# Kernel optimization log

Measured on AMD Instinct MI355X. Metric: run time of the kernel, lower is better.

Reference implementation:

```python
import jax, jax.numpy as jnp
import numpy as np

NP_, NG_ = 20000, 5000            # protein / go_annotation node counts
D_FEAT, D_HID, N_CLS = 512, 128, 1000
E_PP, E_PG, E_GP = 240000, 100000, 100000
NEG_SLOPE = -0.2                  # note: the repo default slope is negative
EPS = 1e-12


def _l2norm(x):
    n = jnp.linalg.norm(x, axis=1, keepdims=True)
    return x / jnp.maximum(n, EPS)


def _edge_softmax(logits, dst, n):
    # per-destination-node softmax over incoming edges, per feature channel
    m = jax.ops.segment_max(logits, dst, num_segments=n)
    e = jnp.exp(logits - m[dst])
    s = jax.ops.segment_sum(e, dst, num_segments=n)
    return e / s[dst]


def _type_attn(h_src, h_dst, src, dst, Wl, bl, Wr, br):
    # GCN-normalized aggregation onto dst nodes, then type-level attention logits,
    # broadcast back to edges (copy_u on the reversed relation graph).
    ns, nd = h_src.shape[0], h_dst.shape[0]
    ones = jnp.ones(src.shape[0], dtype=h_src.dtype)
    outdeg = jnp.clip(jax.ops.segment_sum(ones, src, num_segments=ns), 1.0)
    feat = h_src * (outdeg ** -0.5)[:, None]
    rst = jax.ops.segment_sum(feat[src], dst, num_segments=nd)
    indeg = jnp.clip(jax.ops.segment_sum(ones, dst, num_segments=nd), 1.0)
    rst = rst * (indeg ** -0.5)[:, None]
    ea = jax.nn.elu((h_dst @ Wl + bl) + (rst @ Wr + br))  # [nd, D_HID]
    return ea[dst]                                        # [E, D_HID]


def setup_inputs() -> dict:
    key = jax.random.key(0)
    ks = iter(jax.random.split(key, 40))

    def nrm(shape, s=0.05):
        return jax.random.normal(next(ks), shape, dtype=jnp.float32) * s

    def ri(n, hi):
        return jax.random.randint(next(ks), (n,), 0, hi, dtype=jnp.int32)

    zeros = lambda n: jnp.zeros((n,), jnp.float32)
    return dict(
        x_protein=jax.random.normal(next(ks), (NP_, D_FEAT), dtype=jnp.float32),
        x_go=jax.random.normal(next(ks), (NG_, N_CLS), dtype=jnp.float32),
        src_pp=ri(E_PP, NP_), dst_pp=ri(E_PP, NP_),
        src_pg=ri(E_PG, NP_), dst_pg=ri(E_PG, NG_),
        src_gp=ri(E_GP, NG_), dst_gp=ri(E_GP, NP_),
        W1p=nrm((D_FEAT, D_HID)), b1p=zeros(D_HID),
        W1g=nrm((N_CLS, D_HID)), b1g=zeros(D_HID),
        Wl_p=nrm((D_HID, D_HID)), bl_p=zeros(D_HID),
        Wl_g=nrm((D_HID, D_HID)), bl_g=zeros(D_HID),
        Wr_p=nrm((D_HID, D_HID)), br_p=zeros(D_HID),
        Wr_g=nrm((D_HID, D_HID)), br_g=zeros(D_HID),
        Wnl=nrm((D_HID, D_HID)), bnl=zeros(D_HID),
        Wnr=nrm((D_HID, D_HID)), bnr=zeros(D_HID),
        Wfc=nrm((D_HID, N_CLS)), bfc=zeros(N_CLS),
    )


def reference(x_protein, x_go, src_pp, dst_pp, src_pg, dst_pg, src_gp, dst_gp,
              W1p, b1p, W1g, b1g, Wl_p, bl_p, Wl_g, bl_g,
              Wr_p, br_p, Wr_g, br_g, Wnl, bnl, Wnr, bnr, Wfc, bfc):
    # input projection + row-wise l2 norm (dropout disabled / eval mode)
    hp = _l2norm(x_protein @ W1p + b1p)   # [NP, D_HID]
    hg = _l2norm(x_go @ W1g + b1g)        # [NG, D_HID]

    # ---- TypeAttention over each canonical etype ----
    a_pp = _type_attn(hp, hp, src_pp, dst_pp, Wl_p, bl_p, Wr_p, br_p)
    a_pg = _type_attn(hp, hg, src_pg, dst_pg, Wl_g, bl_g, Wr_p, br_p)
    a_gp = _type_attn(hg, hp, src_gp, dst_gp, Wl_p, bl_p, Wr_g, br_g)

    # homogeneous view: proteins [0,NP), go_annotation [NP,NP+NG)
    gsrc = jnp.concatenate([src_pp, src_pg, src_gp + NP_])
    gdst = jnp.concatenate([dst_pp, dst_pg + NP_, dst_gp])
    alpha = jnp.concatenate([a_pp, a_pg, a_gp], axis=0)   # [E, D_HID]
    n = NP_ + NG_
    alpha = _edge_softmax(alpha, gdst, n)

    # ---- NodeAttention on the homogeneous graph ----
    x = jnp.concatenate([hp, hg], axis=0)                 # [N, D_HID]
    hl = (x @ Wnl + bnl)[gsrc]
    hr = (x @ Wnr + bnr)[gdst]
    e = (hl + hr) * alpha
    e = jnp.where(e > 0, e, NEG_SLOPE * e)                # LeakyReLU(slope=-0.2)
    a = _edge_softmax(e, gdst, n)
    h = jax.ops.segment_sum(x[gsrc] * a, gdst, num_segments=n)

    out = h @ Wfc + bfc   # [N, N_CLS]; rows [:NP]=protein, [NP:]=go_annotation
    return out
```

## Files before the change

### kernel.cpp

```cpp
#include <hip/hip_runtime.h>
#include <math.h>

#define NP 20000
#define NG 5000
#define NTOT 25000
#define DF 512
#define NCLS 1000
#define DH 128
#define EPP 240000
#define EPG 100000
#define EGP 100000
#define ETOT 440000

typedef __attribute__((ext_vector_type(8))) __bf16 bf16x8;
typedef __attribute__((ext_vector_type(4))) float f32x4;

__device__ __forceinline__ void gl2lds16(const void* g, void* l) {
    __builtin_amdgcn_global_load_lds(
        (const __attribute__((address_space(1))) unsigned int*)g,
        (__attribute__((address_space(3))) unsigned int*)l, 16, 0, 0);
}

__device__ __forceinline__ float b2f(unsigned short u) {
    union { unsigned int i; float f; } c; c.i = ((unsigned int)u) << 16; return c.f;
}

__global__ void hist_kernel(const int* __restrict__ src_pp, const int* __restrict__ dst_pp,
                            const int* __restrict__ src_pg, const int* __restrict__ dst_pg,
                            const int* __restrict__ src_gp, const int* __restrict__ dst_gp,
                            int* outdeg_pp, int* outdeg_pg, int* outdeg_gp,
                            int* indeg_pp, int* indeg_gp, int* indeg_pg,
                            int* cnt)
{
    int e = blockIdx.x * blockDim.x + threadIdx.x;
    if (e < EPP) {
        int s = src_pp[e], d = dst_pp[e];
        atomicAdd(&outdeg_pp[s], 1); atomicAdd(&indeg_pp[d], 1); atomicAdd(&cnt[d], 1);
    } else if (e < EPP + EPG) {
        int i = e - EPP; int s = src_pg[i], d = dst_pg[i];
        atomicAdd(&outdeg_pg[s], 1); atomicAdd(&indeg_pg[d], 1); atomicAdd(&cnt[NP + d], 1);
    } else if (e < ETOT) {
        int i = e - EPP - EPG; int s = src_gp[i], d = dst_gp[i];
        atomicAdd(&outdeg_gp[s], 1); atomicAdd(&indeg_gp[d], 1); atomicAdd(&cnt[d], 1);
    }
}

__global__ __launch_bounds__(1024) void scan_kernel(const int* __restrict__ cnt, int* __restrict__ row_ptr)
{
    __shared__ int part[1024];
    int t = threadIdx.x;
    const int CH = (NTOT + 1023) / 1024;
    int base = t * CH;
    int s = 0;
    for (int i = 0; i < CH; i++) { int idx = base + i; if (idx < NTOT) s += cnt[idx]; }
    part[t] = s;
    __syncthreads();
    for (int off = 1; off < 1024; off <<= 1) {
        int v = (t >= off) ? part[t - off] : 0;
        __syncthreads();
        part[t] += v;
        __syncthreads();
    }
    int run = (t == 0) ? 0 : part[t - 1];
    for (int i = 0; i < CH; i++) {
        int idx = base + i;
        if (idx < NTOT) { row_ptr[idx] = run; run += cnt[idx]; }
    }
    if (t == 1023) row_ptr[NTOT] = part[1023];
}

__global__ void scatter_kernel(const int* __restrict__ src_pp, const int* __restrict__ dst_pp,
                               const int* __restrict__ src_pg, const int* __restrict__ dst_pg,
                               const int* __restrict__ src_gp, const int* __restrict__ dst_gp,
                               const int* __restrict__ outdeg_pp, const int* __restrict__ outdeg_pg,
                               const int* __restrict__ outdeg_gp,
                               const int* __restrict__ row_ptr, int* fill,
                               int* __restrict__ payload, float* __restrict__ escale)
{
    int e = blockIdx.x * blockDim.x + threadIdx.x;
    int s, d, t; float sc;
    if (e < EPP) {
        s = src_pp[e]; d = dst_pp[e]; t = 0;
        sc = rsqrtf((float)max(outdeg_pp[s], 1));
    } else if (e < EPP + EPG) {
        int i = e - EPP; s = src_pg[i]; d = NP + dst_pg[i]; t = 1;
        sc = rsqrtf((float)max(outdeg_pg[s], 1));
    } else if (e < ETOT) {
        int i = e - EPP - EPG; int sl = src_gp[i]; s = NP + sl; d = dst_gp[i]; t = 2;
        sc = rsqrtf((float)max(outdeg_gp[sl], 1));
    } else return;
    int pos = row_ptr[d] + atomicAdd(&fill[d], 1);
    payload[pos] = s | (t << 16);
    escale[pos] = sc;
}

__global__ __launch_bounds__(256) void conv_x_kernel(const float* __restrict__ xp, const float* __restrict__ xg,
                                                     __bf16* __restrict__ xpb, __bf16* __restrict__ xgb)
{
    long long e = ((long long)blockIdx.x * 256 + threadIdx.x) * 8;
    __bf16 pk[8];
    if (blockIdx.y == 0) {
        if (e >= (long long)20032 * 512) return;
        int row = (int)(e >> 9), k = (int)(e & 511);
        if (row < NP) {
            f32x4 v0 = *(const f32x4*)(xp + (size_t)row * 512 + k);
            f32x4 v1 = *(const f32x4*)(xp + (size_t)row * 512 + k + 4);
#pragma unroll
            for (int i = 0; i < 4; i++) { pk[i] = (__bf16)v0[i]; pk[4 + i] = (__bf16)v1[i]; }
        } else {
#pragma unroll
            for (int i = 0; i < 8; i++) pk[i] = (__bf16)0.f;
        }
        *(bf16x8*)(xpb + e) = *(bf16x8*)pk;
    } else {
        if (e >= (long long)5056 * 1024) return;
        int row = (int)(e >> 10), k = (int)(e & 1023);
        if (row < NG && k + 7 < 1000) {
            f32x4 v0 = *(const f32x4*)(xg + (size_t)row * 1000 + k);
            f32x4 v1 = *(const f32x4*)(xg + (size_t)row * 1000 + k + 4);
#pragma unroll
            for (int i = 0; i < 4; i++) { pk[i] = (__bf16)v0[i]; pk[4 + i] = (__bf16)v1[i]; }
        } else {
#pragma unroll
            for (int i = 0; i < 8; i++) {
                int kk = k + i;
                pk[i] = (__bf16)((row < NG && kk < 1000) ? xg[(size_t)row * 1000 + kk] : 0.f);
            }
        }
        *(bf16x8*)(xgb + e) = *(bf16x8*)pk;
    }
}

__global__ __launch_bounds__(256) void conv_w_kernel(
    const float* W1p, const float* W1g, const float* Wlp, const float* Wrp, const float* Wrg,
    const float* Wnl, const float* Wnr, const float* Wfc,
    __bf16* w1pt, __bf16* w1gt, __bf16* wlpt, __bf16* wrpt, __bf16* wrgt,
    __bf16* wnlt, __bf16* wnrt, __bf16* wfct)
{
    int e = blockIdx.x * 256 + threadIdx.x;
    switch (blockIdx.y) {
    case 0: if (e < 128 * 512)  { int n = e >> 9, k = e & 511;  w1pt[e] = (__bf16)W1p[(size_t)k * 128 + n]; } break;
    case 1: if (e < 128 * 1024) { int n = e >> 10, k = e & 1023; w1gt[e] = (__bf16)(k < 1000 ? W1g[(size_t)k * 128 + n] : 0.f); } break;
    case 2: if (e < 16384) { int n = e >> 7, k = e & 127; wlpt[e] = (__bf16)Wlp[(size_t)k * 128 + n]; } break;
    case 3: if (e < 16384) { int n = e >> 7, k = e & 127; wrpt[e] = (__bf16)Wrp[(size_t)k * 128 + n]; } break;
    case 4: if (e < 16384) { int n = e >> 7, k = e & 127; wrgt[e] = (__bf16)Wrg[(size_t)k * 128 + n]; } break;
    case 5: if (e < 16384) { int n = e >> 7, k = e & 127; wnlt[e] = (__bf16)Wnl[(size_t)k * 128 + n]; } break;
    case 6: if (e < 16384) { int n = e >> 7, k = e & 127; wnrt[e] = (__bf16)Wnr[(size_t)k * 128 + n]; } break;
    case 7: if (e < 1024 * 128) { int n = e >> 7, k = e & 127; wfct[e] = (__bf16)(n < 1000 ? Wfc[(size_t)k * 1000 + n] : 0.f); } break;
    }
}

struct GJob {
    const __bf16* A1; const __bf16* A2;
    const __bf16* B1; const __bf16* B2;
    const float* b1; const float* b2;
    float* O1; float* O2; __bf16* Ob;
    int M, N, Kp, ksteps;
};

template<int ACT, int DUALA, int DUALW, int EMIT>
__global__ __launch_bounds__(256) void gemm_bt(GJob j0, GJob j1, int split)
{
    __shared__ __align__(16) __bf16 As[64 * 32];
    __shared__ __align__(16) __bf16 A2s[DUALA ? 64 * 32 : 8];
    __shared__ __align__(16) __bf16 Bs[128 * 32];
    __shared__ __align__(16) __bf16 B2s[(DUALA || DUALW) ? 128 * 32 : 8];
    __shared__ float part[2][64];

    GJob j; int bx;
    if ((int)blockIdx.x < split) { j = j0; bx = blockIdx.x; }
    else { j = j1; bx = blockIdx.x - split; }

    const int tid = threadIdx.x;
    const int wave = tid >> 6, lane = tid & 63;
    const int wr = wave >> 1, wc = wave & 1;
    const int l15 = lane & 15, lh = lane >> 4;
    const int row0 = bx * 64;
    const int col0 = blockIdx.y * 128;

    const size_t aoff = (size_t)(row0 + (tid >> 2)) * j.Kp + (tid & 3) * 8;
    const size_t boff0 = (size_t)(col0 + (tid >> 2)) * j.Kp + (tid & 3) * 8;
    const size_t boff1 = boff0 + (size_t)64 * j.Kp;
    char* alds  = (char*)As + wave * 1024;
    char* a2lds = (char*)A2s + wave * 1024;
    char* blds0 = (char*)Bs + wave * 1024;
    char* blds1 = (char*)Bs + 4096 + wave * 1024;
    char* b2lds0 = (char*)B2s + wave * 1024;
    char* b2lds1 = (char*)B2s + 4096 + wave * 1024;

    f32x4 acc[2][4], acc2[2][4];
#pragma unroll
    for (int fm = 0; fm < 2; fm++)
#pragma unroll
        for (int fn = 0; fn < 4; fn++) {
            acc[fm][fn] = (f32x4)0.f;
            if (DUALW) acc2[fm][fn] = (f32x4)0.f;
        }

    for (int ks = 0; ks < j.ksteps; ks++) {
        const int k0 = ks * 32;
        __syncthreads();
        gl2lds16(j.A1 + aoff + k0, alds);
        if (DUALA) gl2lds16(j.A2 + aoff + k0, a2lds);
        gl2lds16(j.B1 + boff0 + k0, blds0);
        gl2lds16(j.B1 + boff1 + k0, blds1);
        if (DUALA || DUALW) {
            gl2lds16(j.B2 + boff0 + k0, b2lds0);
            gl2lds16(j.B2 + boff1 + k0, b2lds1);
        }
        __syncthreads();

#pragma unroll
        for (int fm = 0; fm < 2; fm++) {
            bf16x8 a = *(const bf16x8*)&As[(wr * 32 + fm * 16 + l15) * 32 + lh * 8];
            bf16x8 a2;
            if (DUALA) a2 = *(const bf16x8*)&A2s[(wr * 32 + fm * 16 + l15) * 32 + lh * 8];
#pragma unroll
            for (int fn = 0; fn < 4; fn++) {
                bf16x8 b = *(const bf16x8*)&Bs[(wc * 64 + fn * 16 + l15) * 32 + lh * 8];
                acc[fm][fn] = __builtin_amdgcn_mfma_f32_16x16x32_bf16(a, b, acc[fm][fn], 0, 0, 0);
                if (DUALA) {
                    bf16x8 b2 = *(const bf16x8*)&B2s[(wc * 64 + fn * 16 + l15) * 32 + lh * 8];
                    acc[fm][fn] = __builtin_amdgcn_mfma_f32_16x16x32_bf16(a2, b2, acc[fm][fn], 0, 0, 0);
                }
                if (DUALW) {
                    bf16x8 b2 = *(const bf16x8*)&B2s[(wc * 64 + fn * 16 + l15) * 32 + lh * 8];
                    acc2[fm][fn] = __builtin_amdgcn_mfma_f32_16x16x32_bf16(a, b2, acc2[fm][fn], 0, 0, 0);
                }
            }
        }
    }

    float bias[4], bias2[4];
#pragma unroll
    for (int fn = 0; fn < 4; fn++) {
        int col = col0 + wc * 64 + fn * 16 + l15;
        bias[fn] = 0.f; bias2[fn] = 0.f;
        if (col < j.N) {
            bias[fn] = DUALA ? (j.b1[col] + j.b2[col]) : j.b1[col];
            if (DUALW) bias2[fn] = j.b2[col];
        }
    }

    float vv[2][4][4];
#pragma unroll
    for (int fm = 0; fm < 2; fm++)
#pragma unroll
        for (int fn = 0; fn < 4; fn++)
#pragma unroll
            for (int r = 0; r < 4; r++) {
                float v = acc[fm][fn][r] + bias[fn];
                if (ACT == 1) v = v > 0.f ? v : (expf(v) - 1.f);
                vv[fm][fn][r] = v;
            }

    float scale[2][4];
#pragma unroll
    for (int fm = 0; fm < 2; fm++)
#pragma unroll
        for (int r = 0; r < 4; r++) scale[fm][r] = 1.f;

    if (ACT == 2) {
        float s[2][4];
#pragma unroll
        for (int fm = 0; fm < 2; fm++)
#pragma unroll
            for (int r = 0; r < 4; r++) {
                float v = 0.f;
#pragma unroll
                for (int fn = 0; fn < 4; fn++) v += vv[fm][fn][r] * vv[fm][fn][r];
                v += __shfl_xor(v, 1);
                v += __shfl_xor(v, 2);
                v += __shfl_xor(v, 4);
                v += __shfl_xor(v, 8);
                s[fm][r] = v;
            }
        __syncthreads();
        if (l15 == 0) {
#pragma unroll
            for (int fm = 0; fm < 2; fm++)
#pragma unroll
                for (int r = 0; r < 4; r++)
                    part[wc][wr * 32 + fm * 16 + lh * 4 + r] = s[fm][r];
        }
        __syncthreads();
#pragma unroll
        for (int fm = 0; fm < 2; fm++)
#pragma unroll
            for (int r = 0; r < 4; r++) {
                int rl = wr * 32 + fm * 16 + lh * 4 + r;
                float ss = part[0][rl] + part[1][rl];
                scale[fm][r] = 1.f / fmaxf(sqrtf(ss), 1e-12f);
            }
    }

#pragma unroll
    for (int fm = 0; fm < 2; fm++)
#pragma unroll
        for (int fn = 0; fn < 4; fn++)
#pragma unroll
            for (int r = 0; r < 4; r++) {
                int row = row0 + wr * 32 + fm * 16 + lh * 4 + r;
                int col = col0 + wc * 64 + fn * 16 + l15;
                if (row < j.M && col < j.N) {
                    float v = vv[fm][fn][r] * scale[fm][r];
                    if (EMIT != 2) j.O1[(size_t)row * j.N + col] = v;
                    if (EMIT != 0) j.Ob[(size_t)row * j.N + col] = (__bf16)v;
                    if (DUALW) j.O2[(size_t)row * j.N + col] = acc2[fm][fn][r] + bias2[fn];
                }
            }
}

__global__ __launch_bounds__(128) void rst_agg_kernel(const __bf16* __restrict__ x,
                                                      const int* __restrict__ row_ptr,
                                                      const int* __restrict__ payload,
                                                      const float* __restrict__ escale,
                                                      const int* __restrict__ indeg_pp,
                                                      const int* __restrict__ indeg_gp,
                                                      __bf16* __restrict__ rppb, __bf16* __restrict__ rgpb)
{
    int d = blockIdx.x;
    int c = threadIdx.x;
    int beg = row_ptr[d], end = row_ptr[d + 1];
    float spp = 0.f, sgp = 0.f;
    __shared__ int pl[128];
    __shared__ float sc[128];
    const unsigned short* xu = (const unsigned short*)x;
    for (int base = beg; base < end; base += 128) {
        int n = min(128, end - base);
        __syncthreads();
        if (c < n) { pl[c] = payload[base + c]; sc[c] = escale[base + c]; }
        __syncthreads();
        for (int i = 0; i < n; i++) {
            int p = pl[i]; int s = p & 0xFFFF; int t = p >> 16;
            float v = b2f(xu[(size_t)s * DH + c]) * sc[i];
            if (t == 0) spp += v; else sgp += v;
        }
    }
    float ipp = rsqrtf((float)max(indeg_pp[d], 1));
    float igp = rsqrtf((float)max(indeg_gp[d], 1));
    rppb[(size_t)d * DH + c] = (__bf16)(spp * ipp);
    rgpb[(size_t)d * DH + c] = (__bf16)(sgp * igp);
}

__global__ void wa_kernel(const int* __restrict__ indeg_pp, const int* __restrict__ indeg_gp,
                          float* __restrict__ eapp, float* __restrict__ eagp)
{
    int idx = blockIdx.x * blockDim.x + threadIdx.x;
    if (idx >= NP * DH) return;
    int d = idx >> 7;
    int npp = indeg_pp[d], ngp = indeg_gp[d];
    float app = eapp[idx], agp = eagp[idx];
    float wpp = 0.f, wgp = 0.f;
    if (npp > 0 && ngp > 0) {
        float mx = fmaxf(app, agp);
        float epp = __expf(app - mx), egp = __expf(agp - mx);
        float den = (float)npp * epp + (float)ngp * egp;
        wpp = epp / den; wgp = egp / den;
    } else if (npp > 0) wpp = 1.f / (float)npp;
    else if (ngp > 0) wgp = 1.f / (float)ngp;
    eapp[idx] = wpp;
    eagp[idx] = wgp;
}

__global__ __launch_bounds__(128) void node_attn_kernel(const __bf16* __restrict__ x,
                                                        const __bf16* __restrict__ hlb,
                                                        const float* __restrict__ hr,
                                                        const float* __restrict__ wpp_arr, const float* __restrict__ wgp_arr,
                                                        const int* __restrict__ indeg_pg,
                                                        const int* __restrict__ row_ptr, const int* __restrict__ payload,
                                                        __bf16* __restrict__ hb)
{
    int d = blockIdx.x, c = threadIdx.x;
    int beg = row_ptr[d], end = row_ptr[d + 1];
    float hrd = hr[(size_t)d * DH + c];
    float wpp = 0.f, wgp = 0.f;
    if (d < NP) {
        wpp = wpp_arr[(size_t)d * DH + c];
        wgp = wgp_arr[(size_t)d * DH + c];
    } else {
        float wpg = 1.f / (float)max(indeg_pg[d - NP], 1);
        wpp = wpg; wgp = wpg;
    }
    float ssum = 0.f, acc = 0.f;
    __shared__ int pl[128];
    const unsigned short* xu = (const unsigned short*)x;
    const unsigned short* hu = (const unsigned short*)hlb;
    for (int base = beg; base < end; base += 128) {
        int n = min(128, end - base);
        __syncthreads();
        if (c < n) pl[c] = payload[base + c];
        __syncthreads();
        for (int i = 0; i < n; i++) {
            int p = pl[i]; int s = p & 0xFFFF; int t = p >> 16;
            float al = (t == 0) ? wpp : wgp;
            float e = (b2f(hu[(size_t)s * DH + c]) + hrd) * al;
            e = fmaxf(e, -0.2f * e);
            float pw = __expf(e);
            float xv = b2f(xu[(size_t)s * DH + c]);
            ssum += pw;
            acc += pw * xv;
        }
    }
    hb[(size_t)d * DH + c] = (__bf16)((end > beg) ? acc / ssum : 0.f);
}

extern "C" void kernel_launch(void* const* d_in, const int* in_sizes, int n_in,
                              void* d_out, int out_size, void* d_ws, size_t ws_size,
                              hipStream_t stream)
{
    const float* x_protein = (const float*)d_in[0];
    const float* x_go      = (const float*)d_in[1];
    const int* src_pp = (const int*)d_in[2];
    const int* dst_pp = (const int*)d_in[3];
    const int* src_pg = (const int*)d_in[4];
    const int* dst_pg = (const int*)d_in[5];
    const int* src_gp = (const int*)d_in[6];
    const int* dst_gp = (const int*)d_in[7];
    const float* W1p = (const float*)d_in[8];
    const float* b1p = (const float*)d_in[9];
    const float* W1g = (const float*)d_in[10];
    const float* b1g = (const float*)d_in[11];
    const float* Wl_p = (const float*)d_in[12];
    const float* bl_p = (const float*)d_in[13];
    const float* Wr_p = (const float*)d_in[16];
    const float* br_p = (const float*)d_in[17];
    const float* Wr_g = (const float*)d_in[18];
    const float* br_g = (const float*)d_in[19];
    const float* Wnl = (const float*)d_in[20];
    const float* bnl = (const float*)d_in[21];
    const float* Wnr = (const float*)d_in[22];
    const float* bnr = (const float*)d_in[23];
    const float* Wfc = (const float*)d_in[24];
    const float* bfc = (const float*)d_in[25];
    float* out = (float*)d_out;

    size_t off = 0;
    char* base = (char*)d_ws;
    auto alloc = [&](size_t words) { void* p = base + off * 4; off += (words + 7) & ~(size_t)7; return p; };

    __bf16* xb   = (__bf16*)alloc((size_t)25024 * 128 / 2);
    float*  hr   = (float*)alloc((size_t)25000 * 128);
    __bf16* hlb  = (__bf16*)alloc((size_t)25024 * 128 / 2);
    __bf16* rppb = (__bf16*)alloc((size_t)20032 * 128 / 2);
    __bf16* rgpb = (__bf16*)alloc((size_t)20032 * 128 / 2);
    char* R1 = (char*)alloc((size_t)5128192 + 2588672);
    __bf16* xpb = (__bf16*)R1;
    __bf16* xgb = (__bf16*)(R1 + (size_t)20032 * 512 * 2);
    float*  wpp = (float*)R1;
    float*  wgp = wpp + (size_t)20000 * 128;
    __bf16* haggb = (__bf16*)(wgp + (size_t)20000 * 128);
    __bf16* w1pt = (__bf16*)alloc(128 * 512 / 2);
    __bf16* w1gt = (__bf16*)alloc(128 * 1024 / 2);
    __bf16* wlpt = (__bf16*)alloc(128 * 128 / 2);
    __bf16* wrpt = (__bf16*)alloc(128 * 128 / 2);
    __bf16* wrgt = (__bf16*)alloc(128 * 128 / 2);
    __bf16* wnlt = (__bf16*)alloc(128 * 128 / 2);
    __bf16* wnrt = (__bf16*)alloc(128 * 128 / 2);
    __bf16* wfct = (__bf16*)alloc(1024 * 128 / 2);
    int* ibase = (int*)alloc(140000 + 25001 + 440000);
    int* outdeg_pp = ibase;
    int* outdeg_pg = outdeg_pp + NP;
    int* outdeg_gp = outdeg_pg + NP;
    int* indeg_pp  = outdeg_gp + NG;
    int* indeg_gp  = indeg_pp + NP;
    int* indeg_pg  = indeg_gp + NP;
    int* cnt       = indeg_pg + NG;
    int* fill      = cnt + NTOT;
    int* row_ptr   = fill + NTOT;
    int* payload   = row_ptr + NTOT + 1;
    float* escale  = (float*)alloc(440000);

    hipMemsetAsync(ibase, 0, (size_t)140000 * sizeof(int), stream);

    const int EB = (ETOT + 255) / 256;
    hist_kernel<<<EB, 256, 0, stream>>>(src_pp, dst_pp, src_pg, dst_pg, src_gp, dst_gp,
                                        outdeg_pp, outdeg_pg, outdeg_gp,
                                        indeg_pp, indeg_gp, indeg_pg, cnt);
    scan_kernel<<<1, 1024, 0, stream>>>(cnt, row_ptr);
    scatter_kernel<<<EB, 256, 0, stream>>>(src_pp, dst_pp, src_pg, dst_pg, src_gp, dst_gp,
                                           outdeg_pp, outdeg_pg, outdeg_gp,
                                           row_ptr, fill, payload, escale);

    conv_x_kernel<<<dim3(5008, 2), 256, 0, stream>>>(x_protein, x_go, xpb, xgb);
    conv_w_kernel<<<dim3(512, 8), 256, 0, stream>>>(W1p, W1g, Wl_p, Wr_p, Wr_g, Wnl, Wnr, Wfc,
                                                    w1pt, w1gt, wlpt, wrpt, wrgt, wnlt, wnrt, wfct);

    {
        GJob p0 = { xpb, nullptr, w1pt, nullptr, b1p, nullptr, nullptr, nullptr, xb, NP, 128, 512, 16 };
        GJob p1 = { xgb, nullptr, w1gt, nullptr, b1g, nullptr, nullptr, nullptr,
                    xb + (size_t)NP * 128, NG, 128, 1024, 32 };
        gemm_bt<2, 0, 0, 2><<<392, 256, 0, stream>>>(p0, p1, 313);
    }

    rst_agg_kernel<<<NP, 128, 0, stream>>>(xb, row_ptr, payload, escale, indeg_pp, indeg_gp, rppb, rgpb);

    {
        GJob e0 = { xb, rppb, wlpt, wrpt, bl_p, br_p, wpp, nullptr, nullptr, NP, 128, 128, 4 };
        GJob e1 = { xb, rgpb, wlpt, wrgt, bl_p, br_g, wgp, nullptr, nullptr, NP, 128, 128, 4 };
        gemm_bt<1, 1, 0, 0><<<626, 256, 0, stream>>>(e0, e1, 313);
    }

    wa_kernel<<<(NP * DH + 255) / 256, 256, 0, stream>>>(indeg_pp, indeg_gp, wpp, wgp);

    {
        GJob h0 = { xb, nullptr, wnlt, wnrt, bnl, bnr, nullptr, hr, hlb, NTOT, 128, 128, 4 };
        gemm_bt<0, 0, 1, 2><<<391, 256, 0, stream>>>(h0, h0, 1 << 30);
    }

    node_attn_kernel<<<NTOT, 128, 0, stream>>>(xb, hlb, hr, wpp, wgp, indeg_pg, row_ptr, payload, haggb);

    {
        GJob o0 = { haggb, nullptr, wfct, nullptr, bfc, nullptr, out, nullptr, nullptr, NTOT, NCLS, 128, 4 };
        gemm_bt<0, 0, 0, 0><<<dim3(391, 8), 256, 0, stream>>>(o0, o0, 1 << 30);
    }

    (void)in_sizes; (void)n_in; (void)out_size; (void)ws_size;
}
```

Measured before the change: 296.4 us.

## Privatize degree histograms in LDS, pad fill counters, pack edge payload

```diff
diff --git a/kernel.cpp b/kernel.cpp
--- a/kernel.cpp
+++ b/kernel.cpp
@@ -11,6 +11,7 @@
 #define EPG 100000
 #define EGP 100000
 #define ETOT 440000
+#define FS 16
 
 typedef __attribute__((ext_vector_type(8))) __bf16 bf16x8;
 typedef __attribute__((ext_vector_type(4))) float f32x4;
@@ -25,34 +26,52 @@
     union { unsigned int i; float f; } c; c.i = ((unsigned int)u) << 16; return c.f;
 }
 
-__global__ void hist_kernel(const int* __restrict__ src_pp, const int* __restrict__ dst_pp,
-                            const int* __restrict__ src_pg, const int* __restrict__ dst_pg,
-                            const int* __restrict__ src_gp, const int* __restrict__ dst_gp,
-                            int* outdeg_pp, int* outdeg_pg, int* outdeg_gp,
-                            int* indeg_pp, int* indeg_gp, int* indeg_pg,
-                            int* cnt)
-{
-    int e = blockIdx.x * blockDim.x + threadIdx.x;
-    if (e < EPP) {
-        int s = src_pp[e], d = dst_pp[e];
-        atomicAdd(&outdeg_pp[s], 1); atomicAdd(&indeg_pp[d], 1); atomicAdd(&cnt[d], 1);
-    } else if (e < EPP + EPG) {
-        int i = e - EPP; int s = src_pg[i], d = dst_pg[i];
-        atomicAdd(&outdeg_pg[s], 1); atomicAdd(&indeg_pg[d], 1); atomicAdd(&cnt[NP + d], 1);
-    } else if (e < ETOT) {
-        int i = e - EPP - EPG; int s = src_gp[i], d = dst_gp[i];
-        atomicAdd(&outdeg_gp[s], 1); atomicAdd(&indeg_gp[d], 1); atomicAdd(&cnt[d], 1);
-    }
-}
-
-__global__ __launch_bounds__(1024) void scan_kernel(const int* __restrict__ cnt, int* __restrict__ row_ptr)
+__global__ __launch_bounds__(1024) void hist_priv_kernel(
+    const int* __restrict__ src_pp, const int* __restrict__ dst_pp,
+    const int* __restrict__ src_pg, const int* __restrict__ dst_pg,
+    const int* __restrict__ src_gp, const int* __restrict__ dst_gp,
+    int* __restrict__ outdeg_pp, int* __restrict__ indeg_pp,
+    int* __restrict__ outdeg_pg, int* __restrict__ indeg_pg,
+    int* __restrict__ outdeg_gp, int* __restrict__ indeg_gp)
+{
+    __shared__ int bins[10016];
+    const int* idx; int* outarr; int lo, nbins, nedge;
+    switch (blockIdx.y) {
+    case 0: idx = src_pp; outarr = outdeg_pp; lo = 0;     nbins = 10000; nedge = EPP; break;
+    case 1: idx = src_pp; outarr = outdeg_pp; lo = 10000; nbins = 10000; nedge = EPP; break;
+    case 2: idx = dst_pp; outarr = indeg_pp;  lo = 0;     nbins = 10000; nedge = EPP; break;
+    case 3: idx = dst_pp; outarr = indeg_pp;  lo = 10000; nbins = 10000; nedge = EPP; break;
+    case 4: idx = src_pg; outarr = outdeg_pg; lo = 0;     nbins = 10000; nedge = EPG; break;
+    case 5: idx = src_pg; outarr = outdeg_pg; lo = 10000; nbins = 10000; nedge = EPG; break;
+    case 6: idx = dst_pg; outarr = indeg_pg;  lo = 0;     nbins = 5000;  nedge = EPG; break;
+    case 7: idx = src_gp; outarr = outdeg_gp; lo = 0;     nbins = 5000;  nedge = EGP; break;
+    case 8: idx = dst_gp; outarr = indeg_gp;  lo = 0;     nbins = 10000; nedge = EGP; break;
+    default: idx = dst_gp; outarr = indeg_gp; lo = 10000; nbins = 10000; nedge = EGP; break;
+    }
+    for (int i = threadIdx.x; i < nbins; i += 1024) bins[i] = 0;
+    __syncthreads();
+    for (int e = threadIdx.x; e < nedge; e += 1024) {
+        int b = idx[e] - lo;
+        if ((unsigned)b < (unsigned)nbins) atomicAdd(&bins[b], 1);
+    }
+    __syncthreads();
+    for (int i = threadIdx.x; i < nbins; i += 1024) outarr[lo + i] = bins[i];
+}
+
+__global__ __launch_bounds__(1024) void scan_kernel(const int* __restrict__ indeg_pp,
+                                                    const int* __restrict__ indeg_gp,
+                                                    const int* __restrict__ indeg_pg,
+                                                    int* __restrict__ row_ptr)
 {
     __shared__ int part[1024];
     int t = threadIdx.x;
     const int CH = (NTOT + 1023) / 1024;
     int base = t * CH;
+    auto cntf = [&](int idx) -> int {
+        return (idx < NP) ? (indeg_pp[idx] + indeg_gp[idx]) : indeg_pg[idx - NP];
+    };
     int s = 0;
-    for (int i = 0; i < CH; i++) { int idx = base + i; if (idx < NTOT) s += cnt[idx]; }
+    for (int i = 0; i < CH; i++) { int idx = base + i; if (idx < NTOT) s += cntf(idx); }
     part[t] = s;
     __syncthreads();
     for (int off = 1; off < 1024; off <<= 1) {
@@ -64,7 +83,7 @@
     int run = (t == 0) ? 0 : part[t - 1];
     for (int i = 0; i < CH; i++) {
         int idx = base + i;
-        if (idx < NTOT) { row_ptr[idx] = run; run += cnt[idx]; }
+        if (idx < NTOT) { row_ptr[idx] = run; run += cntf(idx); }
     }
     if (t == 1023) row_ptr[NTOT] = part[1023];
 }
@@ -75,7 +94,7 @@
                                const int* __restrict__ outdeg_pp, const int* __restrict__ outdeg_pg,
                                const int* __restrict__ outdeg_gp,
                                const int* __restrict__ row_ptr, int* fill,
-                               int* __restrict__ payload, float* __restrict__ escale)
+                               int2* __restrict__ edata)
 {
     int e = blockIdx.x * blockDim.x + threadIdx.x;
     int s, d, t; float sc;
@@ -89,9 +108,8 @@
         int i = e - EPP - EPG; int sl = src_gp[i]; s = NP + sl; d = dst_gp[i]; t = 2;
         sc = rsqrtf((float)max(outdeg_gp[sl], 1));
     } else return;
-    int pos = row_ptr[d] + atomicAdd(&fill[d], 1);
-    payload[pos] = s | (t << 16);
-    escale[pos] = sc;
+    int pos = row_ptr[d] + atomicAdd(&fill[d * FS], 1);
+    edata[pos] = make_int2(s | (t << 16), __float_as_int(sc));
 }
 
 __global__ __launch_bounds__(256) void conv_x_kernel(const float* __restrict__ xp, const float* __restrict__ xg,
@@ -313,8 +331,7 @@
 
 __global__ __launch_bounds__(128) void rst_agg_kernel(const __bf16* __restrict__ x,
                                                       const int* __restrict__ row_ptr,
-                                                      const int* __restrict__ payload,
-                                                      const float* __restrict__ escale,
+                                                      const int2* __restrict__ edata,
                                                       const int* __restrict__ indeg_pp,
                                                       const int* __restrict__ indeg_gp,
                                                       __bf16* __restrict__ rppb, __bf16* __restrict__ rgpb)
@@ -329,7 +346,7 @@
     for (int base = beg; base < end; base += 128) {
         int n = min(128, end - base);
         __syncthreads();
-        if (c < n) { pl[c] = payload[base + c]; sc[c] = escale[base + c]; }
+        if (c < n) { int2 e2 = edata[base + c]; pl[c] = e2.x; sc[c] = __int_as_float(e2.y); }
         __syncthreads();
         for (int i = 0; i < n; i++) {
             int p = pl[i]; int s = p & 0xFFFF; int t = p >> 16;
@@ -368,7 +385,7 @@
                                                         const float* __restrict__ hr,
                                                         const float* __restrict__ wpp_arr, const float* __restrict__ wgp_arr,
                                                         const int* __restrict__ indeg_pg,
-                                                        const int* __restrict__ row_ptr, const int* __restrict__ payload,
+                                                        const int* __restrict__ row_ptr, const int2* __restrict__ edata,
                                                         __bf16* __restrict__ hb)
 {
     int d = blockIdx.x, c = threadIdx.x;
@@ -389,7 +406,7 @@
     for (int base = beg; base < end; base += 128) {
         int n = min(128, end - base);
         __syncthreads();
-        if (c < n) pl[c] = payload[base + c];
+        if (c < n) pl[c] = edata[base + c].x;
         __syncthreads();
         for (int i = 0; i < n; i++) {
             int p = pl[i]; int s = p & 0xFFFF; int t = p >> 16;
@@ -458,29 +475,25 @@
     __bf16* wnlt = (__bf16*)alloc(128 * 128 / 2);
     __bf16* wnrt = (__bf16*)alloc(128 * 128 / 2);
     __bf16* wfct = (__bf16*)alloc(1024 * 128 / 2);
-    int* ibase = (int*)alloc(140000 + 25001 + 440000);
-    int* outdeg_pp = ibase;
-    int* outdeg_pg = outdeg_pp + NP;
-    int* outdeg_gp = outdeg_pg + NP;
-    int* indeg_pp  = outdeg_gp + NG;
-    int* indeg_gp  = indeg_pp + NP;
-    int* indeg_pg  = indeg_gp + NP;
-    int* cnt       = indeg_pg + NG;
-    int* fill      = cnt + NTOT;
-    int* row_ptr   = fill + NTOT;
-    int* payload   = row_ptr + NTOT + 1;
-    float* escale  = (float*)alloc(440000);
-
-    hipMemsetAsync(ibase, 0, (size_t)140000 * sizeof(int), stream);
-
-    const int EB = (ETOT + 255) / 256;
-    hist_kernel<<<EB, 256, 0, stream>>>(src_pp, dst_pp, src_pg, dst_pg, src_gp, dst_gp,
-                                        outdeg_pp, outdeg_pg, outdeg_gp,
-                                        indeg_pp, indeg_gp, indeg_pg, cnt);
-    scan_kernel<<<1, 1024, 0, stream>>>(cnt, row_ptr);
-    scatter_kernel<<<EB, 256, 0, stream>>>(src_pp, dst_pp, src_pg, dst_pg, src_gp, dst_gp,
-                                           outdeg_pp, outdeg_pg, outdeg_gp,
-                                           row_ptr, fill, payload, escale);
+    int* outdeg_pp = (int*)alloc(NP);
+    int* outdeg_pg = (int*)alloc(NP);
+    int* outdeg_gp = (int*)alloc(NG);
+    int* indeg_pp  = (int*)alloc(NP);
+    int* indeg_gp  = (int*)alloc(NP);
+    int* indeg_pg  = (int*)alloc(NG);
+    int* fill      = (int*)alloc((size_t)NTOT * FS);
+    int* row_ptr   = (int*)alloc(NTOT + 1);
+    int2* edata    = (int2*)alloc((size_t)ETOT * 2);
+
+    hipMemsetAsync(fill, 0, (size_t)NTOT * FS * sizeof(int), stream);
+
+    hist_priv_kernel<<<dim3(1, 10), 1024, 0, stream>>>(
+        src_pp, dst_pp, src_pg, dst_pg, src_gp, dst_gp,
+        outdeg_pp, indeg_pp, outdeg_pg, indeg_pg, outdeg_gp, indeg_gp);
+    scan_kernel<<<1, 1024, 0, stream>>>(indeg_pp, indeg_gp, indeg_pg, row_ptr);
+    scatter_kernel<<<(ETOT + 255) / 256, 256, 0, stream>>>(
+        src_pp, dst_pp, src_pg, dst_pg, src_gp, dst_gp,
+        outdeg_pp, outdeg_pg, outdeg_gp, row_ptr, fill, edata);
 
     conv_x_kernel<<<dim3(5008, 2), 256, 0, stream>>>(x_protein, x_go, xpb, xgb);
     conv_w_kernel<<<dim3(512, 8), 256, 0, stream>>>(W1p, W1g, Wl_p, Wr_p, Wr_g, Wnl, Wnr, Wfc,
@@ -493,7 +506,7 @@
         gemm_bt<2, 0, 0, 2><<<392, 256, 0, stream>>>(p0, p1, 313);
     }
 
-    rst_agg_kernel<<<NP, 128, 0, stream>>>(xb, row_ptr, payload, escale, indeg_pp, indeg_gp, rppb, rgpb);
+    rst_agg_kernel<<<NP, 128, 0, stream>>>(xb, row_ptr, edata, indeg_pp, indeg_gp, rppb, rgpb);
 
     {
         GJob e0 = { xb, rppb, wlpt, wrpt, bl_p, br_p, wpp, nullptr, nullptr, NP, 128, 128, 4 };
@@ -508,7 +521,7 @@
         gemm_bt<0, 0, 1, 2><<<391, 256, 0, stream>>>(h0, h0, 1 << 30);
     }
 
-    node_attn_kernel<<<NTOT, 128, 0, stream>>>(xb, hlb, hr, wpp, wgp, indeg_pg, row_ptr, payload, haggb);
+    node_attn_kernel<<<NTOT, 128, 0, stream>>>(xb, hlb, hr, wpp, wgp, indeg_pg, row_ptr, edata, haggb);
 
     {
         GJob o0 = { haggb, nullptr, wfct, nullptr, bfc, nullptr, out, nullptr, nullptr, NTOT, NCLS, 128, 4 };
```

Measured after the change: 330.7 us. +11.6%, slower.
